# Kernel optimization log

Hardware: AMD Instinct MI355X
Metric: run time of the kernel (lower is better)

Reference implementation:

```python
import jax, jax.numpy as jnp
import numpy as np

NPOINT = 1024
RADIUS = 0.2
NSAMPLE = 32


def setup_inputs() -> dict:
    key = jax.random.key(0)
    ks = jax.random.split(key, 8)
    B, N, C = 8, 8192, 64
    xyz = jax.random.uniform(ks[0], (B, N, 3), dtype=jnp.float32)
    features = jax.random.normal(ks[1], (B, N, C), dtype=jnp.float32)
    c_in = C + 3  # QueryAndGroup concatenates relative xyz with features
    s = 0.05
    w1 = jax.random.normal(ks[2], (c_in, 64), dtype=jnp.float32) * s
    b1 = jnp.zeros((64,), jnp.float32)
    w2 = jax.random.normal(ks[3], (64, 64), dtype=jnp.float32) * s
    b2 = jnp.zeros((64,), jnp.float32)
    w3 = jax.random.normal(ks[4], (64, 128), dtype=jnp.float32) * s
    b3 = jnp.zeros((128,), jnp.float32)
    return {"xyz": xyz, "features": features, "w1": w1, "b1": b1,
            "w2": w2, "b2": b2, "w3": w3, "b3": b3}


def farthest_point_sample(xyz, npoint):
    # xyz: (B, N, 3) -> (B, npoint) int32 indices
    B, N, _ = xyz.shape

    def step(carry, _):
        dist, far = carry
        centroid = jnp.take_along_axis(xyz, far[:, None, None], axis=1)  # (B,1,3)
        d = jnp.sum((xyz - centroid) ** 2, axis=-1)  # (B,N)
        dist = jnp.minimum(dist, d)
        nxt = jnp.argmax(dist, axis=-1).astype(jnp.int32)
        return (dist, nxt), far

    init = (jnp.full((B, N), 1e10, jnp.float32), jnp.zeros((B,), jnp.int32))
    _, idxs = jax.lax.scan(step, init, None, length=npoint)
    return idxs.T  # (B, npoint)


def ball_query(radius, nsample, xyz, new_xyz):
    # returns (B, S, nsample) int32 neighbor indices into N
    sq = jnp.sum((new_xyz[:, :, None, :] - xyz[:, None, :, :]) ** 2, axis=-1)  # (B,S,N)
    B, S, N = sq.shape
    idx = jnp.broadcast_to(jnp.arange(N, dtype=jnp.int32), (B, S, N))
    idx = jnp.where(sq > radius * radius, N, idx)
    idx = jnp.sort(idx, axis=-1)[:, :, :nsample]
    first = idx[:, :, :1]
    idx = jnp.where(idx == N, first, idx)  # pad with first valid index
    return idx


_gather = jax.vmap(lambda pts, idx: pts[idx])  # per-batch fancy gather


def reference(xyz, features, w1, b1, w2, b2, w3, b3):
    fps_idx = farthest_point_sample(xyz, NPOINT)
    new_xyz = _gather(xyz, fps_idx)  # (B, S, 3)
    nbr_idx = ball_query(RADIUS, NSAMPLE, xyz, new_xyz)  # (B, S, K)
    g_xyz = _gather(xyz, nbr_idx) - new_xyz[:, :, None, :]  # (B,S,K,3) relative coords
    g_feat = _gather(features, nbr_idx)  # (B, S, K, C)
    x = jnp.concatenate([g_xyz, g_feat], axis=-1)  # (B, S, K, C+3)
    # shared pointwise MLP (Conv2d 1x1 + ReLU)
    x = jax.nn.relu(x @ w1 + b1)
    x = jax.nn.relu(x @ w2 + b2)
    x = jax.nn.relu(x @ w3 + b3)
    new_features = jnp.max(x, axis=2)  # max-pool over neighbors -> (B, S, 128)
    return new_xyz, jnp.transpose(new_features, (0, 2, 1))  # (B,S,3), (B,128,S)
```

## Files before the change

### kernel.cpp

```cpp
#include <hip/hip_runtime.h>
#include <stdint.h>

#define N_PTS 8192
#define B_SZ 8
#define NPOINT_ 1024
#define NSAMPLE_ 32
#define NPROD 8
#define NCONS 64
#define CWAVES (NCONS * 8)

typedef float __attribute__((ext_vector_type(2))) f32x2;

template <int CTRL>
__device__ __forceinline__ unsigned long long dpp_lexmax(unsigned long long k) {
    int lo = (int)(unsigned)k;
    int hi = (int)(unsigned)(k >> 32);
    int olo = __builtin_amdgcn_update_dpp(lo, lo, CTRL, 0xf, 0xf, false);
    int ohi = __builtin_amdgcn_update_dpp(hi, hi, CTRL, 0xf, 0xf, false);
    unsigned long long ok =
        ((unsigned long long)(unsigned)ohi << 32) | (unsigned)olo;
    return (ok > k) ? ok : k;
}

#define SM_SPTS 0
#define SM_CPAIR 131072
#define SM_W1 0
#define SM_W2 17920
#define SM_W3 34816
#define SM_B1 68608
#define SM_B2 68864
#define SM_B3 69120
#define SM_XB 69632
#define SM_HB 104448
#define SM_NIDX 139264
#define SM_TOTAL 140288

#define W1S 70
#define W2S 66
#define W3S 66

#define WS_ILIST_OFF 512

__global__ __launch_bounds__(512, 2) void fused_kernel(
    const float* __restrict__ xyz, const float* __restrict__ feat,
    const float* __restrict__ w1, const float* __restrict__ b1,
    const float* __restrict__ w2, const float* __restrict__ b2,
    const float* __restrict__ w3, const float* __restrict__ b3,
    float* __restrict__ new_xyz, float* __restrict__ out,
    int* __restrict__ ws) {
    __shared__ __align__(16) char smem[SM_TOTAL];
    const int t = threadIdx.x;
    const int wave = t >> 6, lane = t & 63;
    int* prog = ws;
    int* ilist = ws + WS_ILIST_OFF;

    if (blockIdx.x < NPROD) {
        float4* spts = (float4*)smem;
        unsigned long long* cpair = (unsigned long long*)(smem + SM_CPAIR);
        const int b = blockIdx.x;
        const float* bx = xyz + (size_t)b * N_PTS * 3;
        int* pp = prog + b * 64;

        f32x2 px[8], py[8], pz[8], dst[8];
#pragma unroll
        for (int jj = 0; jj < 8; ++jj) {
            int p0 = t + 512 * (2 * jj);
            int p1 = t + 512 * (2 * jj + 1);
            float x0 = bx[3 * p0 + 0], y0 = bx[3 * p0 + 1], z0 = bx[3 * p0 + 2];
            float x1 = bx[3 * p1 + 0], y1 = bx[3 * p1 + 1], z1 = bx[3 * p1 + 2];
            spts[p0] = make_float4(x0, y0, z0, 0.0f);
            spts[p1] = make_float4(x1, y1, z1, 0.0f);
            px[jj] = f32x2{x0, x1};
            py[jj] = f32x2{y0, y1};
            pz[jj] = f32x2{z0, z1};
            dst[jj] = f32x2{1e10f, 1e10f};
        }
        __syncthreads();

        float cx = bx[0], cy = bx[1], cz = bx[2];
        int hold = 0;

        for (int it = 1; it < NPOINT_; ++it) {
            f32x2 cx2 = f32x2{cx, cx}, cy2 = f32x2{cy, cy}, cz2 = f32x2{cz, cz};
            {
#pragma clang fp contract(off)
#pragma unroll
                for (int jj = 0; jj < 8; ++jj) {
                    f32x2 dx = px[jj] - cx2;
                    f32x2 dy = py[jj] - cy2;
                    f32x2 dz = pz[jj] - cz2;
                    f32x2 d = (dx * dx + dy * dy) + dz * dz;
                    dst[jj] = __builtin_elementwise_min(dst[jj], d);
                }
            }
            f32x2 m01 = __builtin_elementwise_max(dst[0], dst[1]);
            f32x2 m23 = __builtin_elementwise_max(dst[2], dst[3]);
            f32x2 m45 = __builtin_elementwise_max(dst[4], dst[5]);
            f32x2 m67 = __builtin_elementwise_max(dst[6], dst[7]);
            f32x2 m03 = __builtin_elementwise_max(m01, m23);
            f32x2 m47 = __builtin_elementwise_max(m45, m67);
            f32x2 mm = __builtin_elementwise_max(m03, m47);
            float bv = fmaxf(mm.x, mm.y);
            int ljx = 8, ljy = 8;
#pragma unroll
            for (int jj = 7; jj >= 0; --jj) {
                ljx = (dst[jj].x == bv) ? jj : ljx;
                ljy = (dst[jj].y == bv) ? jj : ljy;
            }
            int cand_x = 2 * ljx;
            int cand_y = 2 * ljy + 1;
            int lj = (cand_x < cand_y) ? cand_x : cand_y;
            int idx = (lj << 9) + t;

            unsigned long long key =
                ((unsigned long long)__float_as_uint(bv) << 32) |
                (unsigned)(~idx);
            key = dpp_lexmax<0x111>(key);
            key = dpp_lexmax<0x112>(key);
            key = dpp_lexmax<0x114>(key);
            key = dpp_lexmax<0x118>(key);
            key = dpp_lexmax<0x142>(key);
            key = dpp_lexmax<0x143>(key);

            const int buf = it & 1;
            if (lane == 63) cpair[buf * 8 + wave] = key;
            __syncthreads();

            if ((it & 63) == 0 && t == 0) {
                __hip_atomic_store(pp, it, __ATOMIC_RELAXED,
                                   __HIP_MEMORY_SCOPE_AGENT);
            }

            unsigned long long k = cpair[buf * 8 + (lane & 7)];
            k = dpp_lexmax<0x111>(k);
            k = dpp_lexmax<0x112>(k);
            k = dpp_lexmax<0x114>(k);
            int wi = ~__builtin_amdgcn_readlane((int)(unsigned)k, 7);

            hold = (lane == (it & 63)) ? wi : hold;

            float4 sp = spts[wi];
            cx = sp.x;
            cy = sp.y;
            cz = sp.z;

            if ((it & 63) == 63 && wave == 0) {
                __hip_atomic_store(&ilist[(b << 10) + (it - 63) + lane], hold,
                                   __ATOMIC_RELAXED, __HIP_MEMORY_SCOPE_AGENT);
            }
        }
        __syncthreads();
        if (t == 0) {
            __hip_atomic_store(pp, NPOINT_, __ATOMIC_RELAXED,
                               __HIP_MEMORY_SCOPE_AGENT);
        }
    } else {
        float* lw1T = (float*)(smem + SM_W1);
        float* lw2T = (float*)(smem + SM_W2);
        float* lw3T = (float*)(smem + SM_W3);
        float* lb1 = (float*)(smem + SM_B1);
        float* lb2 = (float*)(smem + SM_B2);
        float* lb3 = (float*)(smem + SM_B3);

        for (int i = t; i < 67 * 64; i += 512) {
            int k = i >> 6, c = i & 63;
            lw1T[c * W1S + k] = w1[i];
        }
        if (t < 64) lw1T[t * W1S + 67] = 0.0f;
        for (int i = t; i < 64 * 64; i += 512) {
            int k = i >> 6, c = i & 63;
            lw2T[c * W2S + k] = w2[i];
        }
        for (int i = t; i < 64 * 128; i += 512) {
            int k = i >> 7, c = i & 127;
            lw3T[c * W3S + k] = w3[i];
        }
        if (t < 64) {
            lb1[t] = b1[t];
            lb2[t] = b2[t];
        }
        if (t < 128) lb3[t] = b3[t];
        __syncthreads();

        float* xw = (float*)(smem + SM_XB) + wave * (16 * 68);
        float* hw = (float*)(smem + SM_HB) + wave * (16 * 68);
        int* nw = (int*)(smem + SM_NIDX) + wave * 32;
        const float* wc1 = lw1T + lane * W1S;
        const float* wc2 = lw2T + lane * W2S;
        const float* wca = lw3T + lane * W3S;
        const float* wcb = lw3T + (lane + 64) * W3S;

        const int widx = (blockIdx.x - NPROD) * 8 + wave;
        for (int cc = widx; cc < B_SZ * NPOINT_; cc += CWAVES) {
            const int s = cc >> 3, b = cc & 7;
            const int g = (b << 10) + s;
            int* pp = prog + b * 64;

            int pv = __hip_atomic_load(pp, __ATOMIC_RELAXED,
                                       __HIP_MEMORY_SCOPE_AGENT);
            while (pv <= s) {
                int d = s - pv;
                if (d >= 128)
                    __builtin_amdgcn_s_sleep(127);
                else if (d >= 32)
                    __builtin_amdgcn_s_sleep(64);
                else
                    __builtin_amdgcn_s_sleep(8);
                pv = __hip_atomic_load(pp, __ATOMIC_RELAXED,
                                       __HIP_MEMORY_SCOPE_AGENT);
            }
            __builtin_amdgcn_fence(__ATOMIC_ACQUIRE, "agent");
            const int cix = __hip_atomic_load(&ilist[g], __ATOMIC_RELAXED,
                                              __HIP_MEMORY_SCOPE_AGENT);
            const float* cp = xyz + ((size_t)b * N_PTS + cix) * 3;
            const float cx = cp[0];
            const float cy = cp[1];
            const float cz = cp[2];
            if (lane < 3)
                new_xyz[g * 3 + lane] = (lane == 0) ? cx : ((lane == 1) ? cy : cz);

            const float* bx = xyz + (size_t)b * N_PTS * 3;
            const float r2 = 0.04f;
            int taken = 0, firstIdx = -1;
            for (int ch = 0; ch < N_PTS / 64 && taken < NSAMPLE_; ++ch) {
                int p = ch * 64 + lane;
                float dxq = __fsub_rn(bx[3 * p + 0], cx);
                float dyq = __fsub_rn(bx[3 * p + 1], cy);
                float dzq = __fsub_rn(bx[3 * p + 2], cz);
                float sq = __fadd_rn(
                    __fadd_rn(__fmul_rn(dxq, dxq), __fmul_rn(dyq, dyq)),
                    __fmul_rn(dzq, dzq));
                bool pred = !(sq > r2);
                unsigned long long mask = __ballot(pred);
                if (mask) {
                    int cnt = __popcll(mask);
                    if (firstIdx < 0) firstIdx = ch * 64 + (__ffsll(mask) - 1);
                    if (pred) {
                        int pos =
                            taken + __popcll(mask & ((1ull << lane) - 1ull));
                        if (pos < NSAMPLE_) nw[pos] = p;
                    }
                    taken += cnt;
                }
            }
            if (lane >= taken && lane < NSAMPLE_) nw[lane] = firstIdx;
            asm volatile("s_waitcnt lgkmcnt(0)" ::: "memory");

            float mo0 = 0.0f, mo1 = 0.0f;
            for (int half = 0; half < 2; ++half) {
                int iis[16];
#pragma unroll
                for (int r = 0; r < 16; ++r) iis[r] = nw[half * 16 + r];
#pragma unroll
                for (int r = 0; r < 16; ++r) {
                    xw[r * 68 + 3 + lane] =
                        feat[((size_t)b * N_PTS + iis[r]) * 64 + lane];
                    if (lane < 3) {
                        float pv2 = xyz[((size_t)b * N_PTS + iis[r]) * 3 + lane];
                        float cv = (lane == 0) ? cx : ((lane == 1) ? cy : cz);
                        xw[r * 68 + lane] = pv2 - cv;
                    }
                    if (lane == 0) xw[r * 68 + 67] = 0.0f;
                }
                f32x2 acc2[16];
                {
                    float bias = lb1[lane];
#pragma unroll
                    for (int r = 0; r < 16; ++r) acc2[r] = f32x2{bias, 0.0f};
                    for (int kk = 0; kk < 68; kk += 4) {
                        f32x2 wA = *(const f32x2*)(wc1 + kk);
                        f32x2 wB = *(const f32x2*)(wc1 + kk + 2);
#pragma unroll
                        for (int r = 0; r < 16; ++r) {
                            float4 xv = *(const float4*)&xw[r * 68 + kk];
                            f32x2 xa = f32x2{xv.x, xv.y};
                            f32x2 xc = f32x2{xv.z, xv.w};
                            acc2[r] = xa * wA + acc2[r];
                            acc2[r] = xc * wB + acc2[r];
                        }
                    }
#pragma unroll
                    for (int r = 0; r < 16; ++r)
                        hw[r * 68 + lane] = fmaxf(acc2[r].x + acc2[r].y, 0.0f);
                }
                {
                    float bias = lb2[lane];
#pragma unroll
                    for (int r = 0; r < 16; ++r) acc2[r] = f32x2{bias, 0.0f};
                    for (int kk = 0; kk < 64; kk += 4) {
                        f32x2 wA = *(const f32x2*)(wc2 + kk);
                        f32x2 wB = *(const f32x2*)(wc2 + kk + 2);
#pragma unroll
                        for (int r = 0; r < 16; ++r) {
                            float4 hv = *(const float4*)&hw[r * 68 + kk];
                            f32x2 xa = f32x2{hv.x, hv.y};
                            f32x2 xc = f32x2{hv.z, hv.w};
                            acc2[r] = xa * wA + acc2[r];
                            acc2[r] = xc * wB + acc2[r];
                        }
                    }
#pragma unroll
                    for (int r = 0; r < 16; ++r)
                        xw[r * 68 + lane] = fmaxf(acc2[r].x + acc2[r].y, 0.0f);
                }
                {
                    f32x2 a2[16], c2[16];
                    float bb0 = lb3[lane], bb1 = lb3[lane + 64];
#pragma unroll
                    for (int r = 0; r < 16; ++r) {
                        a2[r] = f32x2{bb0, 0.0f};
                        c2[r] = f32x2{bb1, 0.0f};
                    }
                    for (int kk = 0; kk < 64; kk += 4) {
                        f32x2 wA0 = *(const f32x2*)(wca + kk);
                        f32x2 wB0 = *(const f32x2*)(wca + kk + 2);
                        f32x2 wA1 = *(const f32x2*)(wcb + kk);
                        f32x2 wB1 = *(const f32x2*)(wcb + kk + 2);
#pragma unroll
                        for (int r = 0; r < 16; ++r) {
                            float4 hv = *(const float4*)&xw[r * 68 + kk];
                            f32x2 xa = f32x2{hv.x, hv.y};
                            f32x2 xc = f32x2{hv.z, hv.w};
                            a2[r] = xa * wA0 + a2[r];
                            a2[r] = xc * wB0 + a2[r];
                            c2[r] = xa * wA1 + c2[r];
                            c2[r] = xc * wB1 + c2[r];
                        }
                    }
#pragma unroll
                    for (int r = 0; r < 16; ++r) {
                        mo0 = fmaxf(mo0, fmaxf(a2[r].x + a2[r].y, 0.0f));
                        mo1 = fmaxf(mo1, fmaxf(c2[r].x + c2[r].y, 0.0f));
                    }
                }
            }
            out[((size_t)b * 128 + lane) * 1024 + s] = mo0;
            out[((size_t)b * 128 + lane + 64) * 1024 + s] = mo1;
        }
    }
}

extern "C" void kernel_launch(void* const* d_in, const int* in_sizes, int n_in,
                              void* d_out, int out_size, void* d_ws,
                              size_t ws_size, hipStream_t stream) {
    const float* xyz = (const float*)d_in[0];
    const float* feat = (const float*)d_in[1];
    const float* w1 = (const float*)d_in[2];
    const float* b1 = (const float*)d_in[3];
    const float* w2 = (const float*)d_in[4];
    const float* b2 = (const float*)d_in[5];
    const float* w3 = (const float*)d_in[6];
    const float* b3 = (const float*)d_in[7];

    float* out_xyz = (float*)d_out;
    float* out_feat = (float*)d_out + B_SZ * NPOINT_ * 3;
    int* ws = (int*)d_ws;

    (void)hipMemsetAsync(d_ws, 0, WS_ILIST_OFF * sizeof(int), stream);
    fused_kernel<<<NPROD + NCONS, 512, 0, stream>>>(
        xyz, feat, w1, b1, w2, b2, w3, b3, out_xyz, out_feat, ws);
}
```

Before: 1.027 ms.

## Run farthest-point sampling on four waves with sixteen point pairs per thread

The FPS producer block now does its work with only 256 of its 512 threads. Each active thread holds 32 points in registers, and the cross-wave argmax reduction runs over 4 waves instead of 8. The idle threads only match the per-iteration barriers. The aim is a cheaper per-iteration barrier and cross-wave reduction on the serial FPS critical path, paid for with more per-thread arithmetic and higher register pressure.

```diff
diff --git a/kernel.cpp b/kernel.cpp
--- a/kernel.cpp
+++ b/kernel.cpp
@@ -61,98 +61,112 @@
         const float* bx = xyz + (size_t)b * N_PTS * 3;
         int* pp = prog + b * 64;
 
-        f32x2 px[8], py[8], pz[8], dst[8];
-#pragma unroll
-        for (int jj = 0; jj < 8; ++jj) {
-            int p0 = t + 512 * (2 * jj);
-            int p1 = t + 512 * (2 * jj + 1);
-            float x0 = bx[3 * p0 + 0], y0 = bx[3 * p0 + 1], z0 = bx[3 * p0 + 2];
-            float x1 = bx[3 * p1 + 0], y1 = bx[3 * p1 + 1], z1 = bx[3 * p1 + 2];
-            spts[p0] = make_float4(x0, y0, z0, 0.0f);
-            spts[p1] = make_float4(x1, y1, z1, 0.0f);
-            px[jj] = f32x2{x0, x1};
-            py[jj] = f32x2{y0, y1};
-            pz[jj] = f32x2{z0, z1};
-            dst[jj] = f32x2{1e10f, 1e10f};
-        }
-        __syncthreads();
-
-        float cx = bx[0], cy = bx[1], cz = bx[2];
-        int hold = 0;
-
-        for (int it = 1; it < NPOINT_; ++it) {
-            f32x2 cx2 = f32x2{cx, cx}, cy2 = f32x2{cy, cy}, cz2 = f32x2{cz, cz};
-            {
+        if (t < 256) {
+            f32x2 px[16], py[16], pz[16], dst[16];
+#pragma unroll
+            for (int jj = 0; jj < 16; ++jj) {
+                int p0 = t + 256 * (2 * jj);
+                int p1 = t + 256 * (2 * jj + 1);
+                float x0 = bx[3 * p0 + 0], y0 = bx[3 * p0 + 1],
+                      z0 = bx[3 * p0 + 2];
+                float x1 = bx[3 * p1 + 0], y1 = bx[3 * p1 + 1],
+                      z1 = bx[3 * p1 + 2];
+                spts[p0] = make_float4(x0, y0, z0, 0.0f);
+                spts[p1] = make_float4(x1, y1, z1, 0.0f);
+                px[jj] = f32x2{x0, x1};
+                py[jj] = f32x2{y0, y1};
+                pz[jj] = f32x2{z0, z1};
+                dst[jj] = f32x2{1e10f, 1e10f};
+            }
+            __syncthreads();
+
+            float cx = bx[0], cy = bx[1], cz = bx[2];
+            int hold = 0;
+
+            for (int it = 1; it < NPOINT_; ++it) {
+                f32x2 cx2 = f32x2{cx, cx}, cy2 = f32x2{cy, cy},
+                      cz2 = f32x2{cz, cz};
+                {
 #pragma clang fp contract(off)
 #pragma unroll
-                for (int jj = 0; jj < 8; ++jj) {
-                    f32x2 dx = px[jj] - cx2;
-                    f32x2 dy = py[jj] - cy2;
-                    f32x2 dz = pz[jj] - cz2;
-                    f32x2 d = (dx * dx + dy * dy) + dz * dz;
-                    dst[jj] = __builtin_elementwise_min(dst[jj], d);
-                }
-            }
-            f32x2 m01 = __builtin_elementwise_max(dst[0], dst[1]);
-            f32x2 m23 = __builtin_elementwise_max(dst[2], dst[3]);
-            f32x2 m45 = __builtin_elementwise_max(dst[4], dst[5]);
-            f32x2 m67 = __builtin_elementwise_max(dst[6], dst[7]);
-            f32x2 m03 = __builtin_elementwise_max(m01, m23);
-            f32x2 m47 = __builtin_elementwise_max(m45, m67);
-            f32x2 mm = __builtin_elementwise_max(m03, m47);
-            float bv = fmaxf(mm.x, mm.y);
-            int ljx = 8, ljy = 8;
-#pragma unroll
-            for (int jj = 7; jj >= 0; --jj) {
-                ljx = (dst[jj].x == bv) ? jj : ljx;
-                ljy = (dst[jj].y == bv) ? jj : ljy;
-            }
-            int cand_x = 2 * ljx;
-            int cand_y = 2 * ljy + 1;
-            int lj = (cand_x < cand_y) ? cand_x : cand_y;
-            int idx = (lj << 9) + t;
-
-            unsigned long long key =
-                ((unsigned long long)__float_as_uint(bv) << 32) |
-                (unsigned)(~idx);
-            key = dpp_lexmax<0x111>(key);
-            key = dpp_lexmax<0x112>(key);
-            key = dpp_lexmax<0x114>(key);
-            key = dpp_lexmax<0x118>(key);
-            key = dpp_lexmax<0x142>(key);
-            key = dpp_lexmax<0x143>(key);
-
-            const int buf = it & 1;
-            if (lane == 63) cpair[buf * 8 + wave] = key;
+                    for (int jj = 0; jj < 16; ++jj) {
+                        f32x2 dx = px[jj] - cx2;
+                        f32x2 dy = py[jj] - cy2;
+                        f32x2 dz = pz[jj] - cz2;
+                        f32x2 d = (dx * dx + dy * dy) + dz * dz;
+                        dst[jj] = __builtin_elementwise_min(dst[jj], d);
+                    }
+                }
+                f32x2 m[8];
+#pragma unroll
+                for (int jj = 0; jj < 8; ++jj)
+                    m[jj] = __builtin_elementwise_max(dst[2 * jj],
+                                                      dst[2 * jj + 1]);
+                f32x2 n0 = __builtin_elementwise_max(m[0], m[1]);
+                f32x2 n1 = __builtin_elementwise_max(m[2], m[3]);
+                f32x2 n2 = __builtin_elementwise_max(m[4], m[5]);
+                f32x2 n3 = __builtin_elementwise_max(m[6], m[7]);
+                f32x2 q0 = __builtin_elementwise_max(n0, n1);
+                f32x2 q1 = __builtin_elementwise_max(n2, n3);
+                f32x2 mm = __builtin_elementwise_max(q0, q1);
+                float bv = fmaxf(mm.x, mm.y);
+                int ljx = 16, ljy = 16;
+#pragma unroll
+                for (int jj = 15; jj >= 0; --jj) {
+                    ljx = (dst[jj].x == bv) ? jj : ljx;
+                    ljy = (dst[jj].y == bv) ? jj : ljy;
+                }
+                int cand_x = 2 * ljx;
+                int cand_y = 2 * ljy + 1;
+                int k32 = (cand_x < cand_y) ? cand_x : cand_y;
+                int idx = (k32 << 8) + t;
+
+                unsigned long long key =
+                    ((unsigned long long)__float_as_uint(bv) << 32) |
+                    (unsigned)(~idx);
+                key = dpp_lexmax<0x111>(key);
+                key = dpp_lexmax<0x112>(key);
+                key = dpp_lexmax<0x114>(key);
+                key = dpp_lexmax<0x118>(key);
+                key = dpp_lexmax<0x142>(key);
+                key = dpp_lexmax<0x143>(key);
+
+                const int buf = it & 1;
+                if (lane == 63) cpair[buf * 8 + wave] = key;
+                __syncthreads();
+
+                if ((it & 63) == 0 && t == 0) {
+                    __hip_atomic_store(pp, it, __ATOMIC_RELAXED,
+                                       __HIP_MEMORY_SCOPE_AGENT);
+                }
+
+                unsigned long long k = cpair[buf * 8 + (lane & 3)];
+                k = dpp_lexmax<0x111>(k);
+                k = dpp_lexmax<0x112>(k);
+                int wi = ~__builtin_amdgcn_readlane((int)(unsigned)k, 3);
+
+                hold = (lane == (it & 63)) ? wi : hold;
+
+                float4 sp = spts[wi];
+                cx = sp.x;
+                cy = sp.y;
+                cz = sp.z;
+
+                if ((it & 63) == 63 && wave == 0) {
+                    __hip_atomic_store(&ilist[(b << 10) + (it - 63) + lane],
+                                       hold, __ATOMIC_RELAXED,
+                                       __HIP_MEMORY_SCOPE_AGENT);
+                }
+            }
             __syncthreads();
-
-            if ((it & 63) == 0 && t == 0) {
-                __hip_atomic_store(pp, it, __ATOMIC_RELAXED,
+            if (t == 0) {
+                __hip_atomic_store(pp, NPOINT_, __ATOMIC_RELAXED,
                                    __HIP_MEMORY_SCOPE_AGENT);
             }
-
-            unsigned long long k = cpair[buf * 8 + (lane & 7)];
-            k = dpp_lexmax<0x111>(k);
-            k = dpp_lexmax<0x112>(k);
-            k = dpp_lexmax<0x114>(k);
-            int wi = ~__builtin_amdgcn_readlane((int)(unsigned)k, 7);
-
-            hold = (lane == (it & 63)) ? wi : hold;
-
-            float4 sp = spts[wi];
-            cx = sp.x;
-            cy = sp.y;
-            cz = sp.z;
-
-            if ((it & 63) == 63 && wave == 0) {
-                __hip_atomic_store(&ilist[(b << 10) + (it - 63) + lane], hold,
-                                   __ATOMIC_RELAXED, __HIP_MEMORY_SCOPE_AGENT);
-            }
-        }
-        __syncthreads();
-        if (t == 0) {
-            __hip_atomic_store(pp, NPOINT_, __ATOMIC_RELAXED,
-                               __HIP_MEMORY_SCOPE_AGENT);
+        } else {
+            __syncthreads();
+            for (int it = 1; it < NPOINT_; ++it) __syncthreads();
+            __syncthreads();
         }
     } else {
         float* lw1T = (float*)(smem + SM_W1);
```

After: 1.042 ms. No clear change (+1.5%).
